# Optimization experiments

Hardware: AMD Instinct MI355X
Metric: run time of the kernel (lower is better)

Reference implementation:

```python
import jax, jax.numpy as jnp
import numpy as np

D = 1024
H = 16
S = 2048
B = 4
DF = 4 * D
EPS = 1e-5


def setup_inputs() -> dict:
    key = jax.random.key(0)
    ks = jax.random.split(key, 12)
    sd = 0.02
    return {
        "x": jax.random.normal(ks[0], (B, S, D), dtype=jnp.float32),
        "Wq": jax.random.normal(ks[1], (D, D), dtype=jnp.float32) * sd,
        "Wk": jax.random.normal(ks[2], (D, D), dtype=jnp.float32) * sd,
        "Wv": jax.random.normal(ks[3], (D, D), dtype=jnp.float32) * sd,
        "Wo": jax.random.normal(ks[4], (D, D), dtype=jnp.float32) * sd,
        "bo": jnp.zeros((D,), dtype=jnp.float32),
        "W1": jax.random.normal(ks[5], (D, DF), dtype=jnp.float32) * sd,
        "b1": jnp.zeros((DF,), dtype=jnp.float32),
        "W2": jax.random.normal(ks[6], (DF, D), dtype=jnp.float32) * sd,
        "b2": jnp.zeros((D,), dtype=jnp.float32),
        "g1": jnp.ones((D,), dtype=jnp.float32),
        "s1": jnp.zeros((D,), dtype=jnp.float32),
        "g2": jnp.ones((D,), dtype=jnp.float32),
        "s2": jnp.zeros((D,), dtype=jnp.float32),
    }


def _gelu(x):
    # tanh approximation exactly as in the torch GELU module
    c = jnp.sqrt(jnp.asarray(2.0 / jnp.pi, dtype=x.dtype))
    return 0.5 * x * (1.0 + jnp.tanh(c * (x + 0.044715 * x ** 3)))


def _layernorm(x, scale, shift):
    mean = jnp.mean(x, axis=-1, keepdims=True)
    var = jnp.var(x, axis=-1, keepdims=True)  # biased, as unbiased=False
    return scale * (x - mean) * jax.lax.rsqrt(var + EPS) + shift


def _attention(x, Wq, Wk, Wv, Wo, bo):
    b, s, d = x.shape
    hd = d // H
    q = (x @ Wq).reshape(b, s, H, hd).transpose(0, 2, 1, 3)  # [b,h,s,hd]
    k = (x @ Wk).reshape(b, s, H, hd).transpose(0, 2, 1, 3)
    v = (x @ Wv).reshape(b, s, H, hd).transpose(0, 2, 1, 3)
    scores = jnp.einsum("bhqd,bhkd->bhqk", q, k) / jnp.sqrt(jnp.asarray(hd, x.dtype))
    mask = jnp.triu(jnp.ones((s, s), dtype=bool), k=1)
    scores = jnp.where(mask, -jnp.inf, scores)
    w = jax.nn.softmax(scores, axis=-1)  # dropout is identity (rate=0 / eval)
    ctx = jnp.einsum("bhqk,bhkd->bhqd", w, v)
    ctx = ctx.transpose(0, 2, 1, 3).reshape(b, s, d)
    return ctx @ Wo + bo


def reference(x, Wq, Wk, Wv, Wo, bo, W1, b1, W2, b2, g1, s1, g2, s2):
    h = x + _attention(_layernorm(x, g1, s1), Wq, Wk, Wv, Wo, bo)
    y = _layernorm(h, g2, s2)
    ff = _gelu(y @ W1 + b1) @ W2 + b2
    return h + ff
```

## Files before the change

kernel.cpp:

```cpp
#include <hip/hip_runtime.h>
#include <hip/hip_bf16.h>

#define DEV __device__ __forceinline__

typedef __bf16 bf16x8 __attribute__((ext_vector_type(8)));
typedef __bf16 bf16x2v __attribute__((ext_vector_type(2)));
typedef float f32x4 __attribute__((ext_vector_type(4)));
typedef float f32x16 __attribute__((ext_vector_type(16)));
typedef unsigned int u32;
typedef unsigned int u32x4 __attribute__((ext_vector_type(4)));
typedef __hip_bfloat16 hbf;

constexpr int Dm = 1024;
constexpr int Hh = 16;
constexpr int Ss = 2048;
constexpr int Bb = 4;
constexpr int DFm = 4096;
constexpr int LDQ = 3072;

DEV unsigned short f2bfu(float f) {
  hbf h = __float2bfloat16(f);
  return __builtin_bit_cast(unsigned short, h);
}

DEV u32 pkbf(float x, float y) {
  bf16x2v v = {(__bf16)x, (__bf16)y};
  return __builtin_bit_cast(u32, v);
}

DEV float gelu_f(float x) {
  return x / (1.f + __expf(-1.5957691216057308f * (x + 0.044715f * x * x * x)));
}

#define GLDS(src, dst)                                                                     \
  __builtin_amdgcn_global_load_lds((const __attribute__((address_space(1))) void*)(src),   \
                                   (__attribute__((address_space(3))) void*)(dst), 16, 0, 0)

__global__ __launch_bounds__(256) void wtrans_kernel(const float* __restrict__ W,
                                                     hbf* __restrict__ Wt, int K, int N) {
  __shared__ float tile[32][33];
  int k0 = blockIdx.x * 32, n0 = blockIdx.y * 32;
  int tx = threadIdx.x & 31, ty = threadIdx.x >> 5;
  for (int r = ty; r < 32; r += 8) tile[r][tx] = W[(size_t)(k0 + r) * N + n0 + tx];
  __syncthreads();
  for (int r = ty; r < 32; r += 8)
    Wt[(size_t)(n0 + r) * K + k0 + tx] = __float2bfloat16(tile[tx][r]);
}

__global__ __launch_bounds__(256) void wtrans4_kernel(const float* __restrict__ W0,
                                                      const float* __restrict__ W1,
                                                      const float* __restrict__ W2,
                                                      const float* __restrict__ W3,
                                                      hbf* __restrict__ D0, hbf* __restrict__ D1,
                                                      hbf* __restrict__ D2, hbf* __restrict__ D3) {
  __shared__ float tile[32][33];
  const int z = blockIdx.z;
  const float* W = z == 0 ? W0 : z == 1 ? W1 : z == 2 ? W2 : W3;
  hbf* Wt = z == 0 ? D0 : z == 1 ? D1 : z == 2 ? D2 : D3;
  int k0 = blockIdx.x * 32, n0 = blockIdx.y * 32;
  int tx = threadIdx.x & 31, ty = threadIdx.x >> 5;
  for (int r = ty; r < 32; r += 8) tile[r][tx] = W[(size_t)(k0 + r) * 1024 + n0 + tx];
  __syncthreads();
  for (int r = ty; r < 32; r += 8)
    Wt[(size_t)(n0 + r) * 1024 + k0 + tx] = __float2bfloat16(tile[tx][r]);
}

__global__ __launch_bounds__(256) void ln_kernel(const float* __restrict__ x,
                                                 const float* __restrict__ g,
                                                 const float* __restrict__ b,
                                                 hbf* __restrict__ y) {
  int row = blockIdx.x;
  int t = threadIdx.x;
  const float4 v = ((const float4*)(x + (size_t)row * Dm))[t];
  float s = v.x + v.y + v.z + v.w;
  float q = v.x * v.x + v.y * v.y + v.z * v.z + v.w * v.w;
#pragma unroll
  for (int off = 32; off > 0; off >>= 1) {
    s += __shfl_down(s, off);
    q += __shfl_down(q, off);
  }
  __shared__ float red[10];
  int wave = t >> 6, lane = t & 63;
  if (lane == 0) { red[wave] = s; red[4 + wave] = q; }
  __syncthreads();
  if (t == 0) {
    float ts = red[0] + red[1] + red[2] + red[3];
    float tq = red[4] + red[5] + red[6] + red[7];
    float mean = ts * (1.f / Dm);
    float var = tq * (1.f / Dm) - mean * mean;
    red[8] = mean;
    red[9] = rsqrtf(var + 1e-5f);
  }
  __syncthreads();
  float mean = red[8], inv = red[9];
  float4 gv = ((const float4*)g)[t];
  float4 bv = ((const float4*)b)[t];
  ushort4 o;
  o.x = f2bfu(gv.x * (v.x - mean) * inv + bv.x);
  o.y = f2bfu(gv.y * (v.y - mean) * inv + bv.y);
  o.z = f2bfu(gv.z * (v.z - mean) * inv + bv.z);
  o.w = f2bfu(gv.w * (v.w - mean) * inv + bv.w);
  ((ushort4*)(y + (size_t)row * Dm))[t] = o;
}

template <int BN, int WM, int WN, int ACT, bool HAS_BIAS, bool HAS_RES, bool OUT_BF16>
__global__ __launch_bounds__(512, 2) void gemm8(const hbf* __restrict__ A,
                                                const hbf* __restrict__ Bt,
                                                void* __restrict__ Cv,
                                                const float* __restrict__ bias,
                                                const float* __restrict__ res,
                                                int M, int N, int K) {
  constexpr int BM = 256;
  constexpr int MR = (BM / WM) / 16, NR = (BN / WN) / 16;
  constexpr int MQ = MR / 2, NQ = NR / 2;
  constexpr int RPA = (BM / WM) / 2;
  constexpr int RPB = (BN / WN) / 2;
  constexpr int ASL = 128 * 64;
  constexpr int BSL = (BN / 2) * 64;
  constexpr int PERBUF = 2 * ASL + 2 * BSL;
  constexpr int ALD = 2;
  constexpr int BLD = BN / 128;
  constexpr int LPI = 2 * ALD + 2 * BLD;

  __shared__ __align__(16) hbf lds[2 * PERBUF];

  const int tid = threadIdx.x;
  const int lane = tid & 63, wave = tid >> 6;
  const int wr = wave / WN, wc = wave % WN;
  const int lr = lane & 15, lg = lane >> 4;

  const int nwg = gridDim.x;
  const int qq = nwg >> 3, rr = nwg & 7;
  const int xcd = blockIdx.x & 7, oidx = blockIdx.x >> 3;
  const int wg = (xcd < rr ? xcd * (qq + 1) : rr * (qq + 1) + (xcd - rr) * qq) + oidx;
  const int ntn = N / BN;
  const int m0 = (wg / ntn) * BM, n0 = (wg % ntn) * BN;

  const hbf* Ab = A + (size_t)m0 * K;
  const hbf* Bb = Bt + (size_t)n0 * K;

  f32x4 acc[MR][NR] = {};

  auto stageA = [&](int mh, int t, int p) {
#pragma unroll
    for (int l = 0; l < ALD; ++l) {
      int ci = l * 512 + tid;
      int r = ci >> 3, c = ci & 7;
      int piece = r / RPA, rl = r % RPA;
      int grow = piece * (BM / WM) + mh * RPA + rl;
      int gk = t * 64 + ((c ^ (r & 7)) << 3);
      GLDS(Ab + (size_t)grow * K + gk, lds + p * PERBUF + mh * ASL + (size_t)ci * 8);
    }
  };
  auto stageB = [&](int nh, int t, int p) {
#pragma unroll
    for (int l = 0; l < BLD; ++l) {
      int ci = l * 512 + tid;
      int r = ci >> 3, c = ci & 7;
      int piece = r / RPB, rl = r % RPB;
      int grow = piece * (BN / WN) + nh * RPB + rl;
      int gk = t * 64 + ((c ^ (r & 7)) << 3);
      GLDS(Bb + (size_t)grow * K + gk, lds + p * PERBUF + 2 * ASL + nh * BSL + (size_t)ci * 8);
    }
  };
  auto ldA = [&](bf16x8 (&af)[MQ][2], int mh, int p) {
    const hbf* base = lds + p * PERBUF + mh * ASL;
#pragma unroll
    for (int i = 0; i < MQ; ++i)
#pragma unroll
      for (int ks = 0; ks < 2; ++ks) {
        int row = wr * RPA + i * 16 + lr;
        int slot = (ks * 4 + lg) ^ (lr & 7);
        af[i][ks] = *(const bf16x8*)(base + (size_t)row * 64 + slot * 8);
      }
  };
  auto ldB = [&](bf16x8 (&bf)[NQ][2], int nh, int p) {
    const hbf* base = lds + p * PERBUF + 2 * ASL + nh * BSL;
#pragma unroll
    for (int j = 0; j < NQ; ++j)
#pragma unroll
      for (int ks = 0; ks < 2; ++ks) {
        int row = wc * RPB + j * 16 + lr;
        int slot = (ks * 4 + lg) ^ (lr & 7);
        bf[j][ks] = *(const bf16x8*)(base + (size_t)row * 64 + slot * 8);
      }
  };

#define SYNC_LGKM()                                        \
  do {                                                     \
    __builtin_amdgcn_s_barrier();                          \
    asm volatile("s_waitcnt lgkmcnt(0)" ::: "memory");     \
    __builtin_amdgcn_sched_barrier(0);                     \
  } while (0)

#define MFMA_Q(av, bv, mh, nh)                                                        \
  do {                                                                                \
    __builtin_amdgcn_s_setprio(1);                                                    \
    _Pragma("unroll") for (int i_ = 0; i_ < MQ; ++i_)                                 \
    _Pragma("unroll") for (int j_ = 0; j_ < NQ; ++j_)                                 \
    _Pragma("unroll") for (int k_ = 0; k_ < 2; ++k_)                                  \
      acc[(mh) * MQ + i_][(nh) * NQ + j_] = __builtin_amdgcn_mfma_f32_16x16x32_bf16(  \
          (av)[i_][k_], (bv)[j_][k_], acc[(mh) * MQ + i_][(nh) * NQ + j_], 0, 0, 0);  \
    __builtin_amdgcn_s_setprio(0);                                                    \
  } while (0)

  stageA(0, 0, 0); stageB(0, 0, 0); stageA(1, 0, 0); stageB(1, 0, 0);
  stageA(0, 1, 1); stageB(0, 1, 1); stageA(1, 1, 1); stageB(1, 1, 1);
  if constexpr (LPI == 8) asm volatile("s_waitcnt vmcnt(8)" ::: "memory");
  else asm volatile("s_waitcnt vmcnt(6)" ::: "memory");
  __builtin_amdgcn_s_barrier();

  const int T = K >> 6;
  for (int t = 0; t < T; ++t) {
    const int p = t & 1;
    bf16x8 a0[MQ][2], a1[MQ][2], b0[NQ][2], b1[NQ][2];
    ldA(a0, 0, p);
    ldB(b0, 0, p);
    if constexpr (MQ * 2 + NQ * 2 == 12) asm volatile("s_waitcnt lgkmcnt(8)" ::: "memory");
    SYNC_LGKM();
    MFMA_Q(a0, b0, 0, 0);
    __builtin_amdgcn_s_barrier();
    ldA(a1, 1, p);
    if (t + 2 < T) stageA(0, t + 2, p);
    SYNC_LGKM();
    MFMA_Q(a1, b0, 1, 0);
    __builtin_amdgcn_s_barrier();
    ldB(b1, 1, p);
    if (t + 2 < T) { stageB(0, t + 2, p); stageA(1, t + 2, p); }
    SYNC_LGKM();
    MFMA_Q(a1, b1, 1, 1);
    __builtin_amdgcn_s_barrier();
    if (t + 2 < T) stageB(1, t + 2, p);
    MFMA_Q(a0, b1, 0, 1);
    if (t + 1 < T) {
      if (t + 2 < T) {
        if constexpr (LPI == 8) asm volatile("s_waitcnt vmcnt(8)" ::: "memory");
        else asm volatile("s_waitcnt vmcnt(6)" ::: "memory");
      } else {
        asm volatile("s_waitcnt vmcnt(0)" ::: "memory");
      }
    }
    __builtin_amdgcn_s_barrier();
  }
#undef SYNC_LGKM
#undef MFMA_Q

#pragma unroll
  for (int mf = 0; mf < MR; ++mf) {
    int row = m0 + wr * (BM / WM) + mf * 16 + lg * 4;
#pragma unroll
    for (int n = 0; n < NR; ++n) {
      int col = n0 + wc * (BN / WN) + n * 16 + lr;
      float bvl = HAS_BIAS ? bias[col] : 0.f;
#pragma unroll
      for (int j = 0; j < 4; ++j) {
        float v = acc[mf][n][j] + bvl;
        if (ACT == 1) v = gelu_f(v);
        if (HAS_RES) v += res[(size_t)(row + j) * N + col];
        if (OUT_BF16) ((hbf*)Cv)[(size_t)(row + j) * N + col] = __float2bfloat16(v);
        else ((float*)Cv)[(size_t)(row + j) * N + col] = v;
      }
    }
  }
}

__global__ __launch_bounds__(256) void vtrans_kernel(const hbf* __restrict__ qkv,
                                                     hbf* __restrict__ vt) {
  __shared__ unsigned short tile[64][65];
  int bh = blockIdx.y, b = bh >> 4, hh = bh & 15;
  int s0 = blockIdx.x * 64;
  int d = threadIdx.x & 63, r0 = threadIdx.x >> 6;
#pragma unroll
  for (int i = 0; i < 16; ++i) {
    int r = r0 * 16 + i;
    tile[d][r] = __builtin_bit_cast(unsigned short,
                                    qkv[(size_t)(b * Ss + s0 + r) * LDQ + 2048 + hh * 64 + d]);
  }
  __syncthreads();
#pragma unroll
  for (int i = 0; i < 16; ++i) {
    int r = r0 * 16 + i;
    vt[(size_t)(bh * 64 + r) * Ss + s0 + d] = __builtin_bit_cast(hbf, tile[r][d]);
  }
}

__global__ __launch_bounds__(256, 3) void attn_kernel(const hbf* __restrict__ qkv,
                                                      const hbf* __restrict__ vt,
                                                      hbf* __restrict__ ctx) {
  __shared__ __align__(16) hbf Ks[2][64 * 64];
  __shared__ __align__(16) hbf Vs[2][64 * 64];

  const int tid = threadIdx.x;
  const int wave = tid >> 6, lane = tid & 63;
  const int l31 = lane & 31, hi = lane >> 5;

  const int gi = blockIdx.x;
  const int g = gi >> 9, rr_ = gi & 511;
  const int bh = rr_ >> 3, j = rr_ & 7;
  const int bx = g ? j : 15 - j;
  const int b = bh >> 4, hh = bh & 15;
  const int q0b = bx * 128;
  const int q0w = q0b + wave * 32;
  const int nsteps = (q0b + 128) >> 6;
  const int my_steps = (q0w + 95) >> 6;

  constexpr float QSCALE = 0.18033688011112042f;
  bf16x8 qf[4];
  {
    const hbf* qrow = qkv + (size_t)(b * Ss + q0w + l31) * LDQ + hh * 64 + hi * 8;
#pragma unroll
    for (int ds = 0; ds < 4; ++ds) {
      bf16x8 t = *(const bf16x8*)(qrow + ds * 16);
#pragma unroll
      for (int e = 0; e < 8; ++e) qf[ds][e] = (__bf16)((float)t[e] * QSCALE);
    }
  }

  const hbf* kbase = qkv + 1024 + (size_t)(b * Ss) * LDQ + hh * 64;
  const hbf* vbase = vt + (size_t)(bh * 64) * Ss;
  const int i0 = tid, i1 = tid + 256;
  const int r0 = i0 >> 3, s0c = (i0 & 7), r1 = i1 >> 3, s1c = (i1 & 7);
  const int c0 = 8 * (s0c ^ (r0 & 7)), c1 = 8 * (s1c ^ (r1 & 7));

  f32x16 ot[2] = {};
  float m_run = -1e30f, l_run = 0.f;

  {
    hbf* kd = &Ks[0][0];
    hbf* vd = &Vs[0][0];
    GLDS(kbase + (size_t)r0 * LDQ + c0, kd + i0 * 8);
    GLDS(kbase + (size_t)r1 * LDQ + c1, kd + i1 * 8);
    GLDS(vbase + (size_t)r0 * Ss + c0, vd + i0 * 8);
    GLDS(vbase + (size_t)r1 * Ss + c1, vd + i1 * 8);
  }
  __syncthreads();

  int buf = 0;
  for (int it = 0; it < nsteps; ++it) {
    const int k0 = it << 6;
    if (it + 1 < nsteps) {
      hbf* kd = &Ks[buf ^ 1][0];
      hbf* vd = &Vs[buf ^ 1][0];
      GLDS(kbase + (size_t)(k0 + 64 + r0) * LDQ + c0, kd + i0 * 8);
      GLDS(kbase + (size_t)(k0 + 64 + r1) * LDQ + c1, kd + i1 * 8);
      GLDS(vbase + (size_t)r0 * Ss + k0 + 64 + c0, vd + i0 * 8);
      GLDS(vbase + (size_t)r1 * Ss + k0 + 64 + c1, vd + i1 * 8);
    }

    if (it < my_steps) {
      const hbf* kt = &Ks[buf][0];
      f32x16 st[2] = {};
#pragma unroll
      for (int c = 0; c < 2; ++c) {
        const int krow = l31 + 32 * c;
        const int kr7 = krow & 7;
#pragma unroll
        for (int ds = 0; ds < 4; ++ds) {
          bf16x8 kf = *(const bf16x8*)(kt + krow * 64 + 8 * ((ds * 2 + hi) ^ kr7));
          st[c] = __builtin_amdgcn_mfma_f32_32x32x16_bf16(kf, qf[ds], st[c], 0, 0, 0);
        }
      }

      if (it == my_steps - 1) {
        const int qg = q0w + l31;
#pragma unroll
        for (int c = 0; c < 2; ++c)
#pragma unroll
          for (int rg = 0; rg < 16; ++rg) {
            int kg = k0 + c * 32 + (rg & 3) + 8 * (rg >> 2) + 4 * hi;
            if (kg > qg) st[c][rg] = -3e38f;
          }
      }

      float mx = -3e38f;
#pragma unroll
      for (int c = 0; c < 2; ++c)
#pragma unroll
        for (int rg = 0; rg < 16; ++rg) mx = fmaxf(mx, st[c][rg]);
      mx = fmaxf(mx, __shfl_xor(mx, 32));
      if (!__all(mx - m_run <= 11.541560327111707f)) {
        float mn = fmaxf(m_run, mx);
        float sc = exp2f(m_run - mn);
        m_run = mn;
        l_run *= sc;
#pragma unroll
        for (int dc = 0; dc < 2; ++dc)
#pragma unroll
          for (int rg = 0; rg < 16; ++rg) ot[dc][rg] *= sc;
      }
      float rs = 0.f;
#pragma unroll
      for (int c = 0; c < 2; ++c)
#pragma unroll
        for (int rg = 0; rg < 16; ++rg) {
          float p = exp2f(st[c][rg] - m_run);
          st[c][rg] = p;
          rs += p;
        }
      rs += __shfl_xor(rs, 32);
      l_run += rs;

      bf16x8 pf[2][2];
#pragma unroll
      for (int c = 0; c < 2; ++c)
#pragma unroll
        for (int ks = 0; ks < 2; ++ks) {
          const int rb = ks * 8;
          u32 a0 = pkbf(st[c][rb + 0], st[c][rb + 1]);
          u32 a1 = pkbf(st[c][rb + 2], st[c][rb + 3]);
          u32 b0 = pkbf(st[c][rb + 4], st[c][rb + 5]);
          u32 b1 = pkbf(st[c][rb + 6], st[c][rb + 7]);
          u32 pa0 = __shfl_xor(a0, 32), pa1 = __shfl_xor(a1, 32);
          u32 pb0 = __shfl_xor(b0, 32), pb1 = __shfl_xor(b1, 32);
          u32x4 f;
          f.x = hi ? pb0 : a0;
          f.y = hi ? pb1 : a1;
          f.z = hi ? b0 : pa0;
          f.w = hi ? b1 : pa1;
          pf[c][ks] = __builtin_bit_cast(bf16x8, f);
        }

      const hbf* vtl = &Vs[buf][0];
#pragma unroll
      for (int dc = 0; dc < 2; ++dc) {
        const int vrow = l31 + 32 * dc;
        const int vr7 = vrow & 7;
#pragma unroll
        for (int c = 0; c < 2; ++c)
#pragma unroll
          for (int ks = 0; ks < 2; ++ks) {
            bf16x8 vf = *(const bf16x8*)(vtl + vrow * 64 + 8 * ((c * 4 + ks * 2 + hi) ^ vr7));
            ot[dc] = __builtin_amdgcn_mfma_f32_32x32x16_bf16(vf, pf[c][ks], ot[dc], 0, 0, 0);
          }
      }
    }

    __syncthreads();
    buf ^= 1;
  }

  const float inv = 1.f / l_run;
  hbf* crow = ctx + (size_t)(b * Ss + q0w + l31) * Dm + hh * 64;
#pragma unroll
  for (int dc = 0; dc < 2; ++dc)
#pragma unroll
    for (int rg = 0; rg < 4; ++rg) {
      ushort4 w;
      w.x = f2bfu(ot[dc][rg * 4 + 0] * inv);
      w.y = f2bfu(ot[dc][rg * 4 + 1] * inv);
      w.z = f2bfu(ot[dc][rg * 4 + 2] * inv);
      w.w = f2bfu(ot[dc][rg * 4 + 3] * inv);
      *(ushort4*)(crow + dc * 32 + rg * 8 + hi * 4) = w;
    }
}

extern "C" void kernel_launch(void* const* d_in, const int* in_sizes, int n_in,
                              void* d_out, int out_size, void* d_ws, size_t ws_size,
                              hipStream_t stream) {
  const float* x  = (const float*)d_in[0];
  const float* Wq = (const float*)d_in[1];
  const float* Wk = (const float*)d_in[2];
  const float* Wv = (const float*)d_in[3];
  const float* Wo = (const float*)d_in[4];
  const float* bo = (const float*)d_in[5];
  const float* W1 = (const float*)d_in[6];
  const float* b1 = (const float*)d_in[7];
  const float* W2 = (const float*)d_in[8];
  const float* b2 = (const float*)d_in[9];
  const float* g1 = (const float*)d_in[10];
  const float* s1 = (const float*)d_in[11];
  const float* g2 = (const float*)d_in[12];
  const float* s2 = (const float*)d_in[13];
  float* out = (float*)d_out;

  char* ws = (char*)d_ws;
  constexpr size_t MB = 1024ull * 1024ull;
  hbf* wqkvT = (hbf*)(ws + 0 * MB);
  hbf* woT   = (hbf*)(ws + 6 * MB);
  hbf* w1T   = (hbf*)(ws + 8 * MB);
  hbf* w2T   = (hbf*)(ws + 16 * MB);
  hbf* xln   = (hbf*)(ws + 24 * MB);
  hbf* ctx   = (hbf*)(ws + 24 * MB);
  hbf* y2    = (hbf*)(ws + 24 * MB);
  hbf* qkvb  = (hbf*)(ws + 40 * MB);
  hbf* vtb   = (hbf*)(ws + 88 * MB);
  hbf* ff1   = (hbf*)(ws + 40 * MB);
  float* hb  = (float*)(ws + 104 * MB);
  (void)ws_size; (void)in_sizes; (void)n_in; (void)out_size;

  const int BS = Bb * Ss;

  wtrans4_kernel<<<dim3(32, 32, 4), 256, 0, stream>>>(Wq, Wk, Wv, Wo,
                                                      wqkvT, wqkvT + 1024 * 1024,
                                                      wqkvT + 2 * 1024 * 1024, woT);
  wtrans_kernel<<<dim3(32, 128), 256, 0, stream>>>(W1, w1T, Dm, DFm);
  wtrans_kernel<<<dim3(128, 32), 256, 0, stream>>>(W2, w2T, DFm, Dm);

  ln_kernel<<<BS, 256, 0, stream>>>(x, g1, s1, xln);

  gemm8<256, 2, 4, 0, false, false, true><<<384, 512, 0, stream>>>(xln, wqkvT, qkvb, nullptr, nullptr, BS, LDQ, Dm);

  vtrans_kernel<<<dim3(Ss / 64, Bb * Hh), 256, 0, stream>>>(qkvb, vtb);

  attn_kernel<<<dim3(1024), 256, 0, stream>>>(qkvb, vtb, ctx);

  gemm8<128, 4, 2, 0, true, true, false><<<256, 512, 0, stream>>>(ctx, woT, hb, bo, x, BS, Dm, Dm);

  ln_kernel<<<BS, 256, 0, stream>>>(hb, g2, s2, y2);

  gemm8<256, 2, 4, 1, true, false, true><<<512, 512, 0, stream>>>(y2, w1T, ff1, b1, nullptr, BS, DFm, Dm);

  gemm8<128, 4, 2, 0, true, true, false><<<256, 512, 0, stream>>>(ff1, w2T, out, b2, hb, BS, Dm, DFm);
}
```

Baseline: 387.3 us.

## Merge weight transposes, store residual in bf16, add two-phase GEMM pipeline

All six weight transposes now run in one launch. The attention-output residual h is stored in bf16 instead of fp32, so the second layernorm and the final GEMM read half the bytes. The BN=128 GEMMs get a two-phase schedule that loads the full A fragment once per k-step. The change also reorders staging in the four-phase loop, adds MFMA priority hints in attention, and uses fast reciprocal in GELU and the softmax normalisation. Rounding the residual to bf16 lowers the precision of the output.

```diff
diff --git a/kernel.cpp b/kernel.cpp
--- a/kernel.cpp
+++ b/kernel.cpp
@@ -23,23 +23,47 @@
   return __builtin_bit_cast(unsigned short, h);
 }
 
+DEV float bfu2f(unsigned short u) { return __builtin_bit_cast(float, (u32)u << 16); }
+
 DEV u32 pkbf(float x, float y) {
   bf16x2v v = {(__bf16)x, (__bf16)y};
   return __builtin_bit_cast(u32, v);
 }
 
 DEV float gelu_f(float x) {
-  return x / (1.f + __expf(-1.5957691216057308f * (x + 0.044715f * x * x * x)));
+  float e = __expf(-1.5957691216057308f * (x + 0.044715f * x * x * x));
+  return x * __builtin_amdgcn_rcpf(1.f + e);
 }
 
 #define GLDS(src, dst)                                                                     \
   __builtin_amdgcn_global_load_lds((const __attribute__((address_space(1))) void*)(src),   \
                                    (__attribute__((address_space(3))) void*)(dst), 16, 0, 0)
 
-__global__ __launch_bounds__(256) void wtrans_kernel(const float* __restrict__ W,
-                                                     hbf* __restrict__ Wt, int K, int N) {
+__global__ __launch_bounds__(256) void wtransall_kernel(
+    const float* __restrict__ Wq, const float* __restrict__ Wk,
+    const float* __restrict__ Wv, const float* __restrict__ Wo,
+    const float* __restrict__ W1, const float* __restrict__ W2,
+    hbf* __restrict__ dqkv, hbf* __restrict__ dwo,
+    hbf* __restrict__ dw1, hbf* __restrict__ dw2) {
   __shared__ float tile[32][33];
-  int k0 = blockIdx.x * 32, n0 = blockIdx.y * 32;
+  const int i = blockIdx.x;
+  const float* W;
+  hbf* Wt;
+  int K, N, k0, n0;
+  if (i < 4096) {
+    int z = i >> 10, j = i & 1023;
+    W = z == 0 ? Wq : z == 1 ? Wk : z == 2 ? Wv : Wo;
+    Wt = z == 3 ? dwo : dqkv + (size_t)z * 1024 * 1024;
+    K = 1024; N = 1024; k0 = (j & 31) * 32; n0 = (j >> 5) * 32;
+  } else if (i < 8192) {
+    int j = i - 4096;
+    W = W1; Wt = dw1; K = 1024; N = 4096;
+    k0 = (j & 31) * 32; n0 = (j >> 5) * 32;
+  } else {
+    int j = i - 8192;
+    W = W2; Wt = dw2; K = 4096; N = 1024;
+    k0 = (j & 127) * 32; n0 = (j >> 7) * 32;
+  }
   int tx = threadIdx.x & 31, ty = threadIdx.x >> 5;
   for (int r = ty; r < 32; r += 8) tile[r][tx] = W[(size_t)(k0 + r) * N + n0 + tx];
   __syncthreads();
@@ -47,31 +71,20 @@
     Wt[(size_t)(n0 + r) * K + k0 + tx] = __float2bfloat16(tile[tx][r]);
 }
 
-__global__ __launch_bounds__(256) void wtrans4_kernel(const float* __restrict__ W0,
-                                                      const float* __restrict__ W1,
-                                                      const float* __restrict__ W2,
-                                                      const float* __restrict__ W3,
-                                                      hbf* __restrict__ D0, hbf* __restrict__ D1,
-                                                      hbf* __restrict__ D2, hbf* __restrict__ D3) {
-  __shared__ float tile[32][33];
-  const int z = blockIdx.z;
-  const float* W = z == 0 ? W0 : z == 1 ? W1 : z == 2 ? W2 : W3;
-  hbf* Wt = z == 0 ? D0 : z == 1 ? D1 : z == 2 ? D2 : D3;
-  int k0 = blockIdx.x * 32, n0 = blockIdx.y * 32;
-  int tx = threadIdx.x & 31, ty = threadIdx.x >> 5;
-  for (int r = ty; r < 32; r += 8) tile[r][tx] = W[(size_t)(k0 + r) * 1024 + n0 + tx];
-  __syncthreads();
-  for (int r = ty; r < 32; r += 8)
-    Wt[(size_t)(n0 + r) * 1024 + k0 + tx] = __float2bfloat16(tile[tx][r]);
-}
-
-__global__ __launch_bounds__(256) void ln_kernel(const float* __restrict__ x,
+template <bool INBF>
+__global__ __launch_bounds__(256) void ln_kernel(const void* __restrict__ xv,
                                                  const float* __restrict__ g,
                                                  const float* __restrict__ b,
                                                  hbf* __restrict__ y) {
   int row = blockIdx.x;
   int t = threadIdx.x;
-  const float4 v = ((const float4*)(x + (size_t)row * Dm))[t];
+  float4 v;
+  if constexpr (INBF) {
+    ushort4 u = ((const ushort4*)((const hbf*)xv + (size_t)row * Dm))[t];
+    v.x = bfu2f(u.x); v.y = bfu2f(u.y); v.z = bfu2f(u.z); v.w = bfu2f(u.w);
+  } else {
+    v = ((const float4*)((const float*)xv + (size_t)row * Dm))[t];
+  }
   float s = v.x + v.y + v.z + v.w;
   float q = v.x * v.x + v.y * v.y + v.z * v.z + v.w * v.w;
 #pragma unroll
@@ -103,12 +116,12 @@
   ((ushort4*)(y + (size_t)row * Dm))[t] = o;
 }
 
-template <int BN, int WM, int WN, int ACT, bool HAS_BIAS, bool HAS_RES, bool OUT_BF16>
+template <int BN, int WM, int WN, int NPH, int ACT, bool HAS_BIAS, int RES, bool OUT_BF16>
 __global__ __launch_bounds__(512, 2) void gemm8(const hbf* __restrict__ A,
                                                 const hbf* __restrict__ Bt,
                                                 void* __restrict__ Cv,
                                                 const float* __restrict__ bias,
-                                                const float* __restrict__ res,
+                                                const void* __restrict__ resv,
                                                 int M, int N, int K) {
   constexpr int BM = 256;
   constexpr int MR = (BM / WM) / 16, NR = (BN / WN) / 16;
@@ -120,7 +133,6 @@
   constexpr int PERBUF = 2 * ASL + 2 * BSL;
   constexpr int ALD = 2;
   constexpr int BLD = BN / 128;
-  constexpr int LPI = 2 * ALD + 2 * BLD;
 
   __shared__ __align__(16) hbf lds[2 * PERBUF];
 
@@ -172,6 +184,18 @@
         int row = wr * RPA + i * 16 + lr;
         int slot = (ks * 4 + lg) ^ (lr & 7);
         af[i][ks] = *(const bf16x8*)(base + (size_t)row * 64 + slot * 8);
+      }
+  };
+  auto ldAfull = [&](bf16x8 (&af)[MR][2], int p) {
+#pragma unroll
+    for (int f = 0; f < MR; ++f)
+#pragma unroll
+      for (int ks = 0; ks < 2; ++ks) {
+        int mh = f >> 1, i = f & 1;
+        const hbf* base = lds + p * PERBUF + mh * ASL;
+        int row = wr * RPA + i * 16 + lr;
+        int slot = (ks * 4 + lg) ^ (lr & 7);
+        af[f][ks] = *(const bf16x8*)(base + (size_t)row * 64 + slot * 8);
       }
   };
   auto ldB = [&](bf16x8 (&bf)[NQ][2], int nh, int p) {
@@ -204,46 +228,82 @@
     __builtin_amdgcn_s_setprio(0);                                                    \
   } while (0)
 
-  stageA(0, 0, 0); stageB(0, 0, 0); stageA(1, 0, 0); stageB(1, 0, 0);
-  stageA(0, 1, 1); stageB(0, 1, 1); stageA(1, 1, 1); stageB(1, 1, 1);
-  if constexpr (LPI == 8) asm volatile("s_waitcnt vmcnt(8)" ::: "memory");
-  else asm volatile("s_waitcnt vmcnt(6)" ::: "memory");
-  __builtin_amdgcn_s_barrier();
+#define MFMA_H(av, bv, nh)                                                            \
+  do {                                                                                \
+    __builtin_amdgcn_s_setprio(1);                                                    \
+    _Pragma("unroll") for (int f_ = 0; f_ < MR; ++f_)                                 \
+    _Pragma("unroll") for (int j_ = 0; j_ < NQ; ++j_)                                 \
+    _Pragma("unroll") for (int k_ = 0; k_ < 2; ++k_)                                  \
+      acc[f_][(nh) * NQ + j_] = __builtin_amdgcn_mfma_f32_16x16x32_bf16(              \
+          (av)[f_][k_], (bv)[j_][k_], acc[f_][(nh) * NQ + j_], 0, 0, 0);              \
+    __builtin_amdgcn_s_setprio(0);                                                    \
+  } while (0)
 
   const int T = K >> 6;
-  for (int t = 0; t < T; ++t) {
-    const int p = t & 1;
-    bf16x8 a0[MQ][2], a1[MQ][2], b0[NQ][2], b1[NQ][2];
-    ldA(a0, 0, p);
-    ldB(b0, 0, p);
-    if constexpr (MQ * 2 + NQ * 2 == 12) asm volatile("s_waitcnt lgkmcnt(8)" ::: "memory");
-    SYNC_LGKM();
-    MFMA_Q(a0, b0, 0, 0);
+
+  if constexpr (NPH == 4) {
+    stageA(0, 0, 0); stageB(0, 0, 0); stageA(1, 0, 0); stageB(1, 0, 0);
+    stageA(0, 1, 1); stageB(0, 1, 1); stageA(1, 1, 1); stageB(1, 1, 1);
+    asm volatile("s_waitcnt vmcnt(8)" ::: "memory");
     __builtin_amdgcn_s_barrier();
-    ldA(a1, 1, p);
-    if (t + 2 < T) stageA(0, t + 2, p);
-    SYNC_LGKM();
-    MFMA_Q(a1, b0, 1, 0);
+
+    for (int t = 0; t < T; ++t) {
+      const int p = t & 1;
+      bf16x8 a0[MQ][2], a1[MQ][2], b0[NQ][2], b1[NQ][2];
+      ldA(a0, 0, p);
+      ldB(b0, 0, p);
+      asm volatile("s_waitcnt lgkmcnt(8)" ::: "memory");
+      SYNC_LGKM();
+      MFMA_Q(a0, b0, 0, 0);
+      __builtin_amdgcn_s_barrier();
+      ldA(a1, 1, p);
+      if (t + 2 < T) { stageA(0, t + 2, p); stageB(0, t + 2, p); }
+      SYNC_LGKM();
+      MFMA_Q(a1, b0, 1, 0);
+      __builtin_amdgcn_s_barrier();
+      ldB(b1, 1, p);
+      if (t + 2 < T) stageA(1, t + 2, p);
+      SYNC_LGKM();
+      MFMA_Q(a1, b1, 1, 1);
+      __builtin_amdgcn_s_barrier();
+      if (t + 2 < T) stageB(1, t + 2, p);
+      MFMA_Q(a0, b1, 0, 1);
+      if (t + 1 < T) {
+        if (t + 2 < T) asm volatile("s_waitcnt vmcnt(8)" ::: "memory");
+        else asm volatile("s_waitcnt vmcnt(0)" ::: "memory");
+      }
+      __builtin_amdgcn_s_barrier();
+    }
+  } else {
+    stageA(0, 0, 0); stageA(1, 0, 0); stageB(0, 0, 0); stageB(1, 0, 0);
+    stageA(0, 1, 1); stageA(1, 1, 1); stageB(0, 1, 1);
+    asm volatile("s_waitcnt vmcnt(5)" ::: "memory");
     __builtin_amdgcn_s_barrier();
-    ldB(b1, 1, p);
-    if (t + 2 < T) { stageB(0, t + 2, p); stageA(1, t + 2, p); }
-    SYNC_LGKM();
-    MFMA_Q(a1, b1, 1, 1);
-    __builtin_amdgcn_s_barrier();
-    if (t + 2 < T) stageB(1, t + 2, p);
-    MFMA_Q(a0, b1, 0, 1);
-    if (t + 1 < T) {
-      if (t + 2 < T) {
-        if constexpr (LPI == 8) asm volatile("s_waitcnt vmcnt(8)" ::: "memory");
-        else asm volatile("s_waitcnt vmcnt(6)" ::: "memory");
-      } else {
-        asm volatile("s_waitcnt vmcnt(0)" ::: "memory");
-      }
-    }
-    __builtin_amdgcn_s_barrier();
+
+    for (int t = 0; t < T; ++t) {
+      const int p = t & 1;
+      bf16x8 af[MR][2], b0[NQ][2], b1[NQ][2];
+      ldAfull(af, p);
+      ldB(b0, 0, p);
+      if (t + 1 < T) stageB(1, t + 1, p ^ 1);
+      asm volatile("s_waitcnt lgkmcnt(8)" ::: "memory");
+      SYNC_LGKM();
+      MFMA_H(af, b0, 0);
+      __builtin_amdgcn_s_barrier();
+      ldB(b1, 1, p);
+      if (t + 2 < T) { stageA(0, t + 2, p); stageA(1, t + 2, p); stageB(0, t + 2, p); }
+      SYNC_LGKM();
+      MFMA_H(af, b1, 1);
+      if (t + 1 < T) {
+        if (t + 2 < T) asm volatile("s_waitcnt vmcnt(5)" ::: "memory");
+        else asm volatile("s_waitcnt vmcnt(0)" ::: "memory");
+      }
+      __builtin_amdgcn_s_barrier();
+    }
   }
 #undef SYNC_LGKM
 #undef MFMA_Q
+#undef MFMA_H
 
 #pragma unroll
   for (int mf = 0; mf < MR; ++mf) {
@@ -256,7 +316,10 @@
       for (int j = 0; j < 4; ++j) {
         float v = acc[mf][n][j] + bvl;
         if (ACT == 1) v = gelu_f(v);
-        if (HAS_RES) v += res[(size_t)(row + j) * N + col];
+        if constexpr (RES == 1) v += ((const float*)resv)[(size_t)(row + j) * N + col];
+        else if constexpr (RES == 2)
+          v += bfu2f(__builtin_bit_cast(unsigned short,
+                                        ((const hbf*)resv)[(size_t)(row + j) * N + col]));
         if (OUT_BF16) ((hbf*)Cv)[(size_t)(row + j) * N + col] = __float2bfloat16(v);
         else ((float*)Cv)[(size_t)(row + j) * N + col] = v;
       }
@@ -350,6 +413,7 @@
     if (it < my_steps) {
       const hbf* kt = &Ks[buf][0];
       f32x16 st[2] = {};
+      __builtin_amdgcn_s_setprio(1);
 #pragma unroll
       for (int c = 0; c < 2; ++c) {
         const int krow = l31 + 32 * c;
@@ -360,6 +424,7 @@
           st[c] = __builtin_amdgcn_mfma_f32_32x32x16_bf16(kf, qf[ds], st[c], 0, 0, 0);
         }
       }
+      __builtin_amdgcn_s_setprio(0);
 
       if (it == my_steps - 1) {
         const int qg = q0w + l31;
@@ -421,6 +486,7 @@
         }
 
       const hbf* vtl = &Vs[buf][0];
+      __builtin_amdgcn_s_setprio(1);
 #pragma unroll
       for (int dc = 0; dc < 2; ++dc) {
         const int vrow = l31 + 32 * dc;
@@ -433,13 +499,14 @@
             ot[dc] = __builtin_amdgcn_mfma_f32_32x32x16_bf16(vf, pf[c][ks], ot[dc], 0, 0, 0);
           }
       }
+      __builtin_amdgcn_s_setprio(0);
     }
 
     __syncthreads();
     buf ^= 1;
   }
 
-  const float inv = 1.f / l_run;
+  const float inv = __builtin_amdgcn_rcpf(l_run);
   hbf* crow = ctx + (size_t)(b * Ss + q0w + l31) * Dm + hh * 64;
 #pragma unroll
   for (int dc = 0; dc < 2; ++dc)
@@ -485,30 +552,27 @@
   hbf* qkvb  = (hbf*)(ws + 40 * MB);
   hbf* vtb   = (hbf*)(ws + 88 * MB);
   hbf* ff1   = (hbf*)(ws + 40 * MB);
-  float* hb  = (float*)(ws + 104 * MB);
+  hbf* hbb   = (hbf*)(ws + 104 * MB);
   (void)ws_size; (void)in_sizes; (void)n_in; (void)out_size;
 
   const int BS = Bb * Ss;
 
-  wtrans4_kernel<<<dim3(32, 32, 4), 256, 0, stream>>>(Wq, Wk, Wv, Wo,
-                                                      wqkvT, wqkvT + 1024 * 1024,
-                                                      wqkvT + 2 * 1024 * 1024, woT);
-  wtrans_kernel<<<dim3(32, 128), 256, 0, stream>>>(W1, w1T, Dm, DFm);
-  wtrans_kernel<<<dim3(128, 32), 256, 0, stream>>>(W2, w2T, DFm, Dm);
-
-  ln_kernel<<<BS, 256, 0, stream>>>(x, g1, s1, xln);
-
-  gemm8<256, 2, 4, 0, false, false, true><<<384, 512, 0, stream>>>(xln, wqkvT, qkvb, nullptr, nullptr, BS, LDQ, Dm);
+  wtransall_kernel<<<12288, 256, 0, stream>>>(Wq, Wk, Wv, Wo, W1, W2,
+                                              wqkvT, woT, w1T, w2T);
+
+  ln_kernel<false><<<BS, 256, 0, stream>>>(x, g1, s1, xln);
+
+  gemm8<256, 2, 4, 4, 0, false, 0, true><<<384, 512, 0, stream>>>(xln, wqkvT, qkvb, nullptr, nullptr, BS, LDQ, Dm);
 
   vtrans_kernel<<<dim3(Ss / 64, Bb * Hh), 256, 0, stream>>>(qkvb, vtb);
 
   attn_kernel<<<dim3(1024), 256, 0, stream>>>(qkvb, vtb, ctx);
 
-  gemm8<128, 4, 2, 0, true, true, false><<<256, 512, 0, stream>>>(ctx, woT, hb, bo, x, BS, Dm, Dm);
-
-  ln_kernel<<<BS, 256, 0, stream>>>(hb, g2, s2, y2);
-
-  gemm8<256, 2, 4, 1, true, false, true><<<512, 512, 0, stream>>>(y2, w1T, ff1, b1, nullptr, BS, DFm, Dm);
-
-  gemm8<128, 4, 2, 0, true, true, false><<<256, 512, 0, stream>>>(ff1, w2T, out, b2, hb, BS, Dm, DFm);
-}
+  gemm8<128, 4, 2, 2, 0, true, 1, true><<<256, 512, 0, stream>>>(ctx, woT, hbb, bo, x, BS, Dm, Dm);
+
+  ln_kernel<true><<<BS, 256, 0, stream>>>(hbb, g2, s2, y2);
+
+  gemm8<256, 2, 4, 4, 1, true, 0, true><<<512, 512, 0, stream>>>(y2, w1T, ff1, b1, nullptr, BS, DFm, Dm);
+
+  gemm8<128, 4, 2, 2, 0, true, 2, false><<<256, 512, 0, stream>>>(ff1, w2T, out, b2, hbb, BS, Dm, DFm);
+}
```

After: 370.2 us. -4.4%, faster.
